# Kernel tuning notes

Measured on AMD Instinct MI355X. Metric: run time of the kernel, lower is better.

## Reference

```python
import jax, jax.numpy as jnp
import numpy as np

NUM_EXPERTS = 8
TOP_K = 2
HIDDEN = 2048
INTER = 7168
B, S = 4, 2048


def setup_inputs() -> dict:
    key = jax.random.key(0)
    k0, k1, k2, k3, k4 = jax.random.split(key, 5)
    scale_h = 1.0 / np.sqrt(HIDDEN)
    scale_i = 1.0 / np.sqrt(INTER)
    return {
        "hidden_states": jax.random.normal(k0, (B, S, HIDDEN), dtype=jnp.float32),
        "gate_w": jax.random.normal(k1, (NUM_EXPERTS, HIDDEN), dtype=jnp.float32) * scale_h,
        "w1": jax.random.normal(k2, (NUM_EXPERTS, INTER, HIDDEN), dtype=jnp.float32) * scale_h,
        "w3": jax.random.normal(k3, (NUM_EXPERTS, INTER, HIDDEN), dtype=jnp.float32) * scale_h,
        "w2": jax.random.normal(k4, (NUM_EXPERTS, HIDDEN, INTER), dtype=jnp.float32) * scale_i,
    }


def reference(hidden_states, gate_w, w1, w3, w2):
    orig_shape = hidden_states.shape
    x = hidden_states.reshape(-1, HIDDEN)              # [T, H]

    # Router: gate linear -> softmax -> top-k -> renormalize.
    router_logits = x @ gate_w.T                       # [T, E]
    probs = jax.nn.softmax(router_logits, axis=-1)
    topk_w, topk_idx = jax.lax.top_k(probs, TOP_K)     # [T, K]
    topk_w = topk_w / jnp.sum(topk_w, axis=-1, keepdims=True)

    # Dense combine weights: [T, E] with top-k renormalized weights scattered.
    combine = jnp.sum(
        jax.nn.one_hot(topk_idx, NUM_EXPERTS, dtype=x.dtype) * topk_w[..., None],
        axis=1,
    )                                                   # [T, E]

    out = jnp.zeros_like(x)
    # Fixed small loop over experts (structurally distinct weight matrices);
    # avoids materializing a [T, E, I] intermediate.
    for e in range(NUM_EXPERTS):
        g = jax.nn.silu(x @ w1[e].T)                   # [T, I]
        u = x @ w3[e].T                                # [T, I]
        y = (g * u) @ w2[e].T                          # [T, H]
        out = out + combine[:, e:e + 1] * y

    return out.reshape(orig_shape)
```

## Files before the change

kernel.cpp:

```cpp
#include <hip/hip_runtime.h>
#include <stdint.h>

#define NE    8
#define HID   2048
#define INTER 7168
#define TTOK  8192
#define NT1   (HID / 64)
#define NT2   (INTER / 64)

typedef __bf16 bf16;
typedef bf16 bf16x4 __attribute__((ext_vector_type(4)));
typedef bf16 bf16x8 __attribute__((ext_vector_type(8)));
typedef float f32x4 __attribute__((ext_vector_type(4)));

__device__ __forceinline__ void glds16(const void* g, void* l) {
  __builtin_amdgcn_global_load_lds((__attribute__((address_space(1))) void*)g,
                                   (__attribute__((address_space(3))) void*)l, 16, 0, 0);
}

__global__ void cvtrt_kernel(const float* __restrict__ w1, const float* __restrict__ w3,
                             bf16* __restrict__ wdst,
                             const float* __restrict__ x, const float* __restrict__ gw,
                             bf16* __restrict__ xb,
                             int* __restrict__ topk_e, float* __restrict__ topk_w) {
  const long SEG = (long)NE * INTER * HID;
  if (blockIdx.x < 8192) {
    const int seg = blockIdx.x >> 12;
    const int bid = blockIdx.x & 4095;
    const float* src = seg ? w3 : w1;
    bf16* d = wdst + (size_t)seg * SEG;
    long i = (long)bid * blockDim.x + threadIdx.x;
    const long stride = (long)4096 * blockDim.x;
    for (long j = i * 4; j < SEG; j += stride * 4) {
      float4 v = *(const float4*)(src + j);
      bf16x4 o = {(bf16)v.x, (bf16)v.y, (bf16)v.z, (bf16)v.w};
      *(bf16x4*)(d + j) = o;
    }
    return;
  }
  const int rb = blockIdx.x - 8192;
  const int wid = threadIdx.x >> 6, lane = threadIdx.x & 63;
  const int t = rb * 4 + wid;
  if (t >= TTOK) return;
  const float* xr = x + (size_t)t * HID;
  bf16* xw = xb + (size_t)t * HID;
  float xv[32];
#pragma unroll
  for (int i = 0; i < 32; ++i) xv[i] = xr[lane + 64 * i];
#pragma unroll
  for (int i = 0; i < 32; ++i) xw[lane + 64 * i] = (bf16)xv[i];
  float lg[NE];
#pragma unroll
  for (int e = 0; e < NE; ++e) {
    const float* g = gw + e * HID;
    float s = 0.f;
#pragma unroll
    for (int i = 0; i < 32; ++i) s += xv[i] * g[lane + 64 * i];
#pragma unroll
    for (int off = 32; off; off >>= 1) s += __shfl_down(s, off);
    lg[e] = s;
  }
  if (lane == 0) {
    int i1 = 0;
#pragma unroll
    for (int e = 1; e < NE; ++e) if (lg[e] > lg[i1]) i1 = e;
    int i2 = (i1 == 0) ? 1 : 0;
#pragma unroll
    for (int e = 0; e < NE; ++e) if (e != i2 && e != i1 && lg[e] > lg[i2]) i2 = e;
    float r = __expf(lg[i2] - lg[i1]);
    float wa = 1.f / (1.f + r);
    topk_e[2 * t] = i1; topk_e[2 * t + 1] = i2;
    topk_w[2 * t] = wa; topk_w[2 * t + 1] = 1.f - wa;
  }
}

__global__ void gather_sorted(const int* __restrict__ topk_e, const float* __restrict__ topk_w,
                              int* __restrict__ cnt, int* __restrict__ ltok,
                              float* __restrict__ lw, int* __restrict__ ppos) {
  const int e = blockIdx.x;
  const int tid = threadIdx.x;
  const int lane = tid & 63, wv = tid >> 6;
  __shared__ int wtot[4];
  __shared__ int basesh;
  if (tid == 0) basesh = 0;
  __syncthreads();
  for (int c0 = 0; c0 < TTOK; c0 += 256) {
    const int t = c0 + tid;
    const int e0 = topk_e[2 * t], e1 = topk_e[2 * t + 1];
    const int j = (e0 == e) ? 0 : 1;
    const int flag = (e0 == e) || (e1 == e);
    unsigned long long b = __ballot(flag);
    int wrank = __popcll(b & ((1ULL << lane) - 1ULL));
    if (lane == 63) wtot[wv] = __popcll(b);
    __syncthreads();
    int wbase = 0;
#pragma unroll
    for (int k = 0; k < 4; ++k) if (k < wv) wbase += wtot[k];
    const int total = wtot[0] + wtot[1] + wtot[2] + wtot[3];
    const int pos = basesh + wbase + wrank;
    if (flag) {
      ltok[e * TTOK + pos] = t;
      lw[e * TTOK + pos] = (j == 0) ? topk_w[2 * t] : topk_w[2 * t + 1];
      ppos[2 * t + j] = pos;
    }
    __syncthreads();
    if (tid == 0) basesh += total;
    __syncthreads();
  }
  if (tid == 0) cnt[e] = basesh;
}

__global__ void combine_kernel(const bf16* __restrict__ ybuf, const int* __restrict__ topk_e,
                               const int* __restrict__ ppos, const int* __restrict__ cnt,
                               float* __restrict__ out) {
  __shared__ int pref[NE];
  if (threadIdx.x < NE) {
    int b = 0;
    for (int k = 0; k < (int)threadIdx.x; ++k) b += cnt[k];
    pref[threadIdx.x] = b;
  }
  __syncthreads();
  const int t = blockIdx.x;
  const int col = threadIdx.x * 8;
  const int g0 = pref[topk_e[2 * t]] + ppos[2 * t];
  const int g1 = pref[topk_e[2 * t + 1]] + ppos[2 * t + 1];
  bf16x8 y0 = *(const bf16x8*)(ybuf + (size_t)g0 * HID + col);
  bf16x8 y1 = *(const bf16x8*)(ybuf + (size_t)g1 * HID + col);
  float4 o0, o1;
  o0.x = (float)y0[0] + (float)y1[0]; o0.y = (float)y0[1] + (float)y1[1];
  o0.z = (float)y0[2] + (float)y1[2]; o0.w = (float)y0[3] + (float)y1[3];
  o1.x = (float)y0[4] + (float)y1[4]; o1.y = (float)y0[5] + (float)y1[5];
  o1.z = (float)y0[6] + (float)y1[6]; o1.w = (float)y0[7] + (float)y1[7];
  float4* o = (float4*)(out + (size_t)t * HID + col);
  o[0] = o0; o[1] = o1;
}


#define MFMA(a, b, c) __builtin_amdgcn_mfma_f32_16x16x32_bf16((a), (b), (c), 0, 0, 0)

#define STAGE_A(h, kt) do { int _b = ((kt) & 1) * 32768; size_t _k = (size_t)(kt) * 128; \
    glds16(bA + oA[(h)*2 + 0] + _k, ldsA + _b + (h) * 16384 + d0); \
    glds16(bA + oA[(h)*2 + 1] + _k, ldsA + _b + (h) * 16384 + d1); } while (0)
#define STAGE_B(h, kt) do { int _b = ((kt) & 1) * 32768; size_t _k = (size_t)(kt) * 128; \
    glds16(bB + oB[(h)*2 + 0] + _k, ldsB + _b + (h) * 16384 + d0); \
    glds16(bB + oB[(h)*2 + 1] + _k, ldsB + _b + (h) * 16384 + d1); } while (0)

#define RD_A(mf, ks) (*(const bf16x8*)(ldsA + curb + arow + (mf) * (16 * 128) + ((ks) ? kcol1 : kcol0)))
#define RD_B(nf, ks) (*(const bf16x8*)(ldsB + curb + brow + (nf) * (16 * 128) + ((ks) ? kcol1 : kcol0)))

#define BAR()    __builtin_amdgcn_s_barrier()
#define LGKMC(n) do { asm volatile("s_waitcnt lgkmcnt(" #n ")" ::: "memory"); \
                      __builtin_amdgcn_sched_barrier(0); } while (0)
#define SCHED0() __builtin_amdgcn_sched_barrier(0)

#define Q_MFMA(AM, BM, ACCM, ACCN_OFF) do { \
  __builtin_amdgcn_s_setprio(1); \
  _Pragma("unroll") \
  for (int m = 0; m < 4; ++m) \
    _Pragma("unroll") \
    for (int n = 0; n < 2; ++n) { \
      acc[ACCM + m][ACCN_OFF + n] = MFMA(AM[m][0], BM[n][0], acc[ACCM + m][ACCN_OFF + n]); \
      acc[ACCM + m][ACCN_OFF + n] = MFMA(AM[m][1], BM[n][1], acc[ACCM + m][ACCN_OFF + n]); \
    } \
  __builtin_amdgcn_s_setprio(0); \
} while (0)

__launch_bounds__(512, 2)
__global__ void pass1_kernel(const bf16* __restrict__ xb, const bf16* __restrict__ w1b,
                             const float* __restrict__ w2f, bf16* __restrict__ w2b,
                             bf16* __restrict__ hbuf, const int* __restrict__ cnt,
                             const int* __restrict__ ltok) {
  if (blockIdx.z == NE) {
    const long n4 = (long)NE * HID * INTER / 4;
    long i = (long)(blockIdx.y * gridDim.x + blockIdx.x) * blockDim.x + threadIdx.x;
    const long stride = (long)gridDim.x * gridDim.y * blockDim.x;
    const float4* src = (const float4*)w2f;
    bf16x4* dst = (bf16x4*)w2b;
    for (long j = i; j < n4; j += stride) {
      float4 v = src[j];
      bf16x4 o = {(bf16)v.x, (bf16)v.y, (bf16)v.z, (bf16)v.w};
      dst[j] = o;
    }
    return;
  }
  const int e = blockIdx.z;
  const int c = cnt[e];
  const int tm = blockIdx.y;
  if (tm * 256 >= c) return;
  const int tn = blockIdx.x;
  int be = 0;
#pragma unroll
  for (int k = 0; k < NE; ++k) if (k < e) be += cnt[k];

  __shared__ __align__(16) bf16 sA[2][256 * 64];
  __shared__ __align__(16) bf16 sB[2][256 * 64];
  char* const ldsA = (char*)&sA[0][0];
  char* const ldsB = (char*)&sB[0][0];

  const int tid = threadIdx.x;
  const int r0 = tid >> 3;
  const int ls = (tid & 7) ^ (r0 & 7);
  const int d0 = tid * 16, d1 = (tid + 512) * 16;
  const char* const bA = (const char*)xb;
  const char* const bB = (const char*)w1b;

  uint32_t oA[4], oB[4];
#pragma unroll
  for (int i = 0; i < 4; ++i) {
    int slot = tm * 256 + i * 64 + r0; if (slot >= c) slot = c - 1;
    oA[i] = (uint32_t)((size_t)ltok[e * TTOK + slot] * (HID * 2) + ls * 16);
    int br = i * 64 + r0;
    int w = (br >> 4) & 1;
    int wr = tn * 128 + ((br >> 5) << 4) + (br & 15);
    size_t off = ((size_t)e * INTER + wr) * (HID * 2) + (size_t)ls * 16;
    if (w) off += (size_t)NE * INTER * HID * 2;
    oB[i] = (uint32_t)off;
  }

  const int lane = tid & 63, wid = tid >> 6;
  const int wm = wid >> 2, wn = wid & 3;
  const int ln15 = lane & 15, kq = lane >> 4;
  const int swz = (ln15 & 7) << 4;
  const int kcol0 = (kq * 16) ^ swz;
  const int kcol1 = (64 + kq * 16) ^ swz;
  const int arow = (wm * 128 + ln15) * 128;
  const int brow = (wn * 64 + ln15) * 128;

  f32x4 acc[8][4];
#pragma unroll
  for (int m = 0; m < 8; ++m)
#pragma unroll
    for (int n = 0; n < 4; ++n) acc[m][n] = (f32x4){0.f, 0.f, 0.f, 0.f};

  STAGE_A(0, 0); STAGE_A(1, 0); STAGE_B(0, 0); STAGE_B(1, 0);
  asm volatile("s_waitcnt vmcnt(4)" ::: "memory");
  STAGE_A(0, 1); STAGE_A(1, 1); STAGE_B(0, 1);
  asm volatile("s_waitcnt vmcnt(6)" ::: "memory");
  BAR();

  bf16x8 a0[4][2], a1[4][2], b0[2][2], b1[2][2];
  int cur = 0;
  for (int t = 0; t < NT1; ++t, cur ^= 1) {
    const int curb = cur * 32768;
#pragma unroll
    for (int m = 0; m < 4; ++m) { a0[m][0] = RD_A(m, 0); a0[m][1] = RD_A(m, 1); }
#pragma unroll
    for (int n = 0; n < 2; ++n) { b0[n][0] = RD_B(n, 0); b0[n][1] = RD_B(n, 1); }
    if (t + 1 < NT1) STAGE_B(1, t + 1);
    BAR(); LGKMC(12);
    if (t > 0) Q_MFMA(a1, b1, 4, 2);
    BAR();
#pragma unroll
    for (int m = 0; m < 4; ++m) { a1[m][0] = RD_A(4 + m, 0); a1[m][1] = RD_A(4 + m, 1); }
    BAR(); LGKMC(8);
    Q_MFMA(a0, b0, 0, 0);
    BAR();
#pragma unroll
    for (int n = 0; n < 2; ++n) { b1[n][0] = RD_B(2 + n, 0); b1[n][1] = RD_B(2 + n, 1); }
    if (t + 2 < NT1) { STAGE_A(0, t + 2); STAGE_A(1, t + 2); SCHED0(); }
    BAR(); LGKMC(4);
    Q_MFMA(a1, b0, 4, 0);
    BAR();
    if (t + 2 < NT1) STAGE_B(0, t + 2);
    LGKMC(0);
    Q_MFMA(a0, b1, 0, 2);
    if (t + 2 < NT1) asm volatile("s_waitcnt vmcnt(6)" ::: "memory");
    else             asm volatile("s_waitcnt vmcnt(0)" ::: "memory");
    BAR();
  }
  Q_MFMA(a1, b1, 4, 2);

#pragma unroll
  for (int mh = 0; mh < 2; ++mh)
#pragma unroll
    for (int mf = 0; mf < 4; ++mf)
#pragma unroll
      for (int j = 0; j < 4; ++j) {
        const int slot = tm * 256 + wm * 128 + mh * 64 + mf * 16 + kq * 4 + j;
        if (slot < c) {
          bf16* hrow = hbuf + (size_t)(be + slot) * INTER + tn * 128;
#pragma unroll
          for (int p = 0; p < 2; ++p) {
            const float g = acc[mh * 4 + mf][2 * p][j];
            const float u = acc[mh * 4 + mf][2 * p + 1][j];
            const float hv = g / (1.f + __expf(-g)) * u;
            hrow[wn * 32 + p * 16 + ln15] = (bf16)hv;
          }
        }
      }
}

__launch_bounds__(512, 2)
__global__ void pass2_kernel(const bf16* __restrict__ hbuf, const bf16* __restrict__ w2b,
                             bf16* __restrict__ ybuf, const int* __restrict__ cnt,
                             const float* __restrict__ lw) {
  const int e = blockIdx.z;
  const int c = cnt[e];
  const int tm = blockIdx.y;
  if (tm * 256 >= c) return;
  const int tn = blockIdx.x;
  int be = 0;
#pragma unroll
  for (int k = 0; k < NE; ++k) if (k < e) be += cnt[k];

  __shared__ __align__(16) bf16 sA[2][256 * 64];
  __shared__ __align__(16) bf16 sB[2][256 * 64];
  char* const ldsA = (char*)&sA[0][0];
  char* const ldsB = (char*)&sB[0][0];

  const int tid = threadIdx.x;
  const int r0 = tid >> 3;
  const int ls = (tid & 7) ^ (r0 & 7);
  const int d0 = tid * 16, d1 = (tid + 512) * 16;
  const char* const bA = (const char*)hbuf;
  const char* const bB = (const char*)w2b;

  uint32_t oA[4], oB[4];
#pragma unroll
  for (int i = 0; i < 4; ++i) {
    int slot = tm * 256 + i * 64 + r0; if (slot >= c) slot = c - 1;
    oA[i] = (uint32_t)((size_t)(be + slot) * (INTER * 2) + ls * 16);
    oB[i] = (uint32_t)(((size_t)e * HID + tn * 256 + i * 64 + r0) * (INTER * 2) + (size_t)ls * 16);
  }

  const int lane = tid & 63, wid = tid >> 6;
  const int wm = wid >> 2, wn = wid & 3;
  const int ln15 = lane & 15, kq = lane >> 4;
  const int swz = (ln15 & 7) << 4;
  const int kcol0 = (kq * 16) ^ swz;
  const int kcol1 = (64 + kq * 16) ^ swz;
  const int arow = (wm * 128 + ln15) * 128;
  const int brow = (wn * 64 + ln15) * 128;

  f32x4 acc[8][4];
#pragma unroll
  for (int m = 0; m < 8; ++m)
#pragma unroll
    for (int n = 0; n < 4; ++n) acc[m][n] = (f32x4){0.f, 0.f, 0.f, 0.f};

  STAGE_A(0, 0); STAGE_A(1, 0); STAGE_B(0, 0); STAGE_B(1, 0);
  asm volatile("s_waitcnt vmcnt(4)" ::: "memory");
  STAGE_A(0, 1); STAGE_A(1, 1); STAGE_B(0, 1);
  asm volatile("s_waitcnt vmcnt(6)" ::: "memory");
  BAR();

  bf16x8 a0[4][2], a1[4][2], b0[2][2], b1[2][2];
  int cur = 0;
  for (int t = 0; t < NT2; ++t, cur ^= 1) {
    const int curb = cur * 32768;
#pragma unroll
    for (int m = 0; m < 4; ++m) { a0[m][0] = RD_A(m, 0); a0[m][1] = RD_A(m, 1); }
#pragma unroll
    for (int n = 0; n < 2; ++n) { b0[n][0] = RD_B(n, 0); b0[n][1] = RD_B(n, 1); }
    if (t + 1 < NT2) STAGE_B(1, t + 1);
    BAR(); LGKMC(12);
    if (t > 0) Q_MFMA(a1, b1, 4, 2);
    BAR();
#pragma unroll
    for (int m = 0; m < 4; ++m) { a1[m][0] = RD_A(4 + m, 0); a1[m][1] = RD_A(4 + m, 1); }
    BAR(); LGKMC(8);
    Q_MFMA(a0, b0, 0, 0);
    BAR();
#pragma unroll
    for (int n = 0; n < 2; ++n) { b1[n][0] = RD_B(2 + n, 0); b1[n][1] = RD_B(2 + n, 1); }
    if (t + 2 < NT2) { STAGE_A(0, t + 2); STAGE_A(1, t + 2); SCHED0(); }
    BAR(); LGKMC(4);
    Q_MFMA(a1, b0, 4, 0);
    BAR();
    if (t + 2 < NT2) STAGE_B(0, t + 2);
    LGKMC(0);
    Q_MFMA(a0, b1, 0, 2);
    if (t + 2 < NT2) asm volatile("s_waitcnt vmcnt(6)" ::: "memory");
    else             asm volatile("s_waitcnt vmcnt(0)" ::: "memory");
    BAR();
  }
  Q_MFMA(a1, b1, 4, 2);

#pragma unroll
  for (int mh = 0; mh < 2; ++mh)
#pragma unroll
    for (int mf = 0; mf < 4; ++mf)
#pragma unroll
      for (int j = 0; j < 4; ++j) {
        const int slot = tm * 256 + wm * 128 + mh * 64 + mf * 16 + kq * 4 + j;
        if (slot < c) {
          const float wt = lw[e * TTOK + slot];
          bf16* yrow = ybuf + (size_t)(be + slot) * HID + tn * 256;
#pragma unroll
          for (int n = 0; n < 4; ++n)
            yrow[wn * 64 + n * 16 + ln15] = (bf16)(wt * acc[mh * 4 + mf][n][j]);
        }
      }
}

extern "C" void kernel_launch(void* const* d_in, const int* in_sizes, int n_in,
                              void* d_out, int out_size, void* d_ws, size_t ws_size,
                              hipStream_t stream) {
  const float* x  = (const float*)d_in[0];
  const float* gw = (const float*)d_in[1];
  const float* w1 = (const float*)d_in[2];
  const float* w3 = (const float*)d_in[3];
  const float* w2 = (const float*)d_in[4];
  float* out = (float*)d_out;

  char* ws = (char*)d_ws;
  size_t off = 0;
  auto take = [&](size_t bytes) -> char* {
    char* p = ws + off;
    off += (bytes + 255) & ~(size_t)255;
    return p;
  };
  bf16* xb    = (bf16*)take((size_t)TTOK * HID * 2);
  bf16* w1b   = (bf16*)take((size_t)NE * INTER * HID * 2);
  bf16* w3b   = (bf16*)take((size_t)NE * INTER * HID * 2);
  bf16* w2b   = (bf16*)take((size_t)NE * HID * INTER * 2);
  bf16* hbuf  = (bf16*)take((size_t)TTOK * 2 * INTER * 2);
  bf16* ybuf  = (bf16*)take((size_t)TTOK * 2 * HID * 2);
  int*   topk_e = (int*)take(TTOK * 2 * 4);
  float* topk_w = (float*)take(TTOK * 2 * 4);
  int*   ltok   = (int*)take(NE * TTOK * 4);
  float* lwgt   = (float*)take(NE * TTOK * 4);
  int*   ppos   = (int*)take(TTOK * 2 * 4);
  int*   cntp   = (int*)take(64);
  if (off > ws_size) return;
  (void)w3b;

  cvtrt_kernel<<<8192 + TTOK / 4, 256, 0, stream>>>(w1, w3, w1b, x, gw, xb, topk_e, topk_w);
  gather_sorted<<<NE, 256, 0, stream>>>(topk_e, topk_w, cntp, ltok, lwgt, ppos);

  pass1_kernel<<<dim3(INTER / 128, TTOK / 256, NE + 1), 512, 0, stream>>>(
      xb, w1b, w2, w2b, hbuf, cntp, ltok);
  pass2_kernel<<<dim3(HID / 256, TTOK / 256, NE), 512, 0, stream>>>(
      hbuf, w2b, ybuf, cntp, lwgt);
  combine_kernel<<<TTOK, 256, 0, stream>>>(ybuf, topk_e, ppos, cntp, out);
}
```

Baseline: 2.105 ms.

## Switch expert GEMMs to 32x32x16 MFMA with k-major LDS layout

Both expert GEMM kernels move from 16x16x32 bf16 MFMA to 32x32x16 bf16 MFMA with 16-wide accumulators. The LDS tile layout becomes k-chunk-major, so each lane reads 16-byte fragments without the XOR swizzle. The main loop becomes a simpler two-phase schedule with full lgkm waits. Larger MFMA tiles aim to cut LDS read traffic per FLOP and instruction count. In exchange, the interleaved multi-phase overlap is gone, and the new layout may cause LDS bank conflicts.

```diff
diff --git a/kernel.cpp b/kernel.cpp
--- a/kernel.cpp
+++ b/kernel.cpp
@@ -11,7 +11,7 @@
 typedef __bf16 bf16;
 typedef bf16 bf16x4 __attribute__((ext_vector_type(4)));
 typedef bf16 bf16x8 __attribute__((ext_vector_type(8)));
-typedef float f32x4 __attribute__((ext_vector_type(4)));
+typedef float f32x16 __attribute__((ext_vector_type(16)));
 
 __device__ __forceinline__ void glds16(const void* g, void* l) {
   __builtin_amdgcn_global_load_lds((__attribute__((address_space(1))) void*)g,
@@ -136,7 +136,7 @@
 }
 
 
-#define MFMA(a, b, c) __builtin_amdgcn_mfma_f32_16x16x32_bf16((a), (b), (c), 0, 0, 0)
+#define MFMA32(a, b, c) __builtin_amdgcn_mfma_f32_32x32x16_bf16((a), (b), (c), 0, 0, 0)
 
 #define STAGE_A(h, kt) do { int _b = ((kt) & 1) * 32768; size_t _k = (size_t)(kt) * 128; \
     glds16(bA + oA[(h)*2 + 0] + _k, ldsA + _b + (h) * 16384 + d0); \
@@ -145,23 +145,23 @@
     glds16(bB + oB[(h)*2 + 0] + _k, ldsB + _b + (h) * 16384 + d0); \
     glds16(bB + oB[(h)*2 + 1] + _k, ldsB + _b + (h) * 16384 + d1); } while (0)
 
-#define RD_A(mf, ks) (*(const bf16x8*)(ldsA + curb + arow + (mf) * (16 * 128) + ((ks) ? kcol1 : kcol0)))
-#define RD_B(nf, ks) (*(const bf16x8*)(ldsB + curb + brow + (nf) * (16 * 128) + ((ks) ? kcol1 : kcol0)))
+#define RD_A(mf, ks) (*(const bf16x8*)(ldsA + curb + aOff + (mf) * 4096 + kcq[ks]))
+#define RD_B(nf, ks) (*(const bf16x8*)(ldsB + curb + bOff + (nf) * 4096 + kcq[ks]))
 
 #define BAR()    __builtin_amdgcn_s_barrier()
-#define LGKMC(n) do { asm volatile("s_waitcnt lgkmcnt(" #n ")" ::: "memory"); \
+#define LGKM0()  do { asm volatile("s_waitcnt lgkmcnt(0)" ::: "memory"); \
                       __builtin_amdgcn_sched_barrier(0); } while (0)
 #define SCHED0() __builtin_amdgcn_sched_barrier(0)
 
-#define Q_MFMA(AM, BM, ACCM, ACCN_OFF) do { \
+#define Q_MFMA32(AM, ACCM) do { \
   __builtin_amdgcn_s_setprio(1); \
   _Pragma("unroll") \
-  for (int m = 0; m < 4; ++m) \
+  for (int ks = 0; ks < 4; ++ks) \
     _Pragma("unroll") \
-    for (int n = 0; n < 2; ++n) { \
-      acc[ACCM + m][ACCN_OFF + n] = MFMA(AM[m][0], BM[n][0], acc[ACCM + m][ACCN_OFF + n]); \
-      acc[ACCM + m][ACCN_OFF + n] = MFMA(AM[m][1], BM[n][1], acc[ACCM + m][ACCN_OFF + n]); \
-    } \
+    for (int m = 0; m < 2; ++m) \
+      _Pragma("unroll") \
+      for (int n = 0; n < 2; ++n) \
+        acc[ACCM + m][n] = MFMA32(AM[m][ks], bF[n][ks], acc[ACCM + m][n]); \
   __builtin_amdgcn_s_setprio(0); \
 } while (0)
 
@@ -198,96 +198,93 @@
   char* const ldsB = (char*)&sB[0][0];
 
   const int tid = threadIdx.x;
-  const int r0 = tid >> 3;
-  const int ls = (tid & 7) ^ (r0 & 7);
   const int d0 = tid * 16, d1 = (tid + 512) * 16;
   const char* const bA = (const char*)xb;
   const char* const bB = (const char*)w1b;
 
   uint32_t oA[4], oB[4];
 #pragma unroll
-  for (int i = 0; i < 4; ++i) {
-    int slot = tm * 256 + i * 64 + r0; if (slot >= c) slot = c - 1;
-    oA[i] = (uint32_t)((size_t)ltok[e * TTOK + slot] * (HID * 2) + ls * 16);
-    int br = i * 64 + r0;
-    int w = (br >> 4) & 1;
-    int wr = tn * 128 + ((br >> 5) << 4) + (br & 15);
-    size_t off = ((size_t)e * INTER + wr) * (HID * 2) + (size_t)ls * 16;
-    if (w) off += (size_t)NE * INTER * HID * 2;
-    oB[i] = (uint32_t)off;
+  for (int j = 0; j < 2; ++j) {
+    const int ch = j ? (tid + 512) : tid;
+    const int g = ch >> 8, q = (ch >> 5) & 7, r = ch & 31;
+#pragma unroll
+    for (int h = 0; h < 2; ++h) {
+      const int rowt = h * 128 + g * 32 + r;
+      int slot = tm * 256 + rowt; if (slot >= c) slot = c - 1;
+      oA[h * 2 + j] = (uint32_t)((size_t)ltok[e * TTOK + slot] * (HID * 2) + q * 16);
+      const int br = rowt;
+      const int w = (br >> 5) & 1;
+      const int wr = tn * 128 + (br >> 6) * 32 + (br & 31);
+      size_t off = ((size_t)e * INTER + wr) * (HID * 2) + (size_t)q * 16;
+      if (w) off += (size_t)NE * INTER * HID * 2;
+      oB[h * 2 + j] = (uint32_t)off;
+    }
   }
 
   const int lane = tid & 63, wid = tid >> 6;
   const int wm = wid >> 2, wn = wid & 3;
-  const int ln15 = lane & 15, kq = lane >> 4;
-  const int swz = (ln15 & 7) << 4;
-  const int kcol0 = (kq * 16) ^ swz;
-  const int kcol1 = (64 + kq * 16) ^ swz;
-  const int arow = (wm * 128 + ln15) * 128;
-  const int brow = (wn * 64 + ln15) * 128;
-
-  f32x4 acc[8][4];
-#pragma unroll
-  for (int m = 0; m < 8; ++m)
-#pragma unroll
-    for (int n = 0; n < 4; ++n) acc[m][n] = (f32x4){0.f, 0.f, 0.f, 0.f};
+  const int ln31 = lane & 31, kq2 = lane >> 5;
+  int kcq[4];
+#pragma unroll
+  for (int ks = 0; ks < 4; ++ks) kcq[ks] = (ks * 2 + kq2) * 512;
+  const int aOff = wm * 16384 + ln31 * 16;
+  const int bOff = (wn >> 1) * 16384 + (wn & 1) * 8192 + ln31 * 16;
+
+  f32x16 acc[4][2];
+#pragma unroll
+  for (int m = 0; m < 4; ++m)
+#pragma unroll
+    for (int n = 0; n < 2; ++n) acc[m][n] = (f32x16)(0.f);
 
   STAGE_A(0, 0); STAGE_A(1, 0); STAGE_B(0, 0); STAGE_B(1, 0);
-  asm volatile("s_waitcnt vmcnt(4)" ::: "memory");
   STAGE_A(0, 1); STAGE_A(1, 1); STAGE_B(0, 1);
   asm volatile("s_waitcnt vmcnt(6)" ::: "memory");
   BAR();
 
-  bf16x8 a0[4][2], a1[4][2], b0[2][2], b1[2][2];
+  bf16x8 aF[2][4], bF[2][4];
   int cur = 0;
   for (int t = 0; t < NT1; ++t, cur ^= 1) {
     const int curb = cur * 32768;
 #pragma unroll
-    for (int m = 0; m < 4; ++m) { a0[m][0] = RD_A(m, 0); a0[m][1] = RD_A(m, 1); }
-#pragma unroll
-    for (int n = 0; n < 2; ++n) { b0[n][0] = RD_B(n, 0); b0[n][1] = RD_B(n, 1); }
-    if (t + 1 < NT1) STAGE_B(1, t + 1);
-    BAR(); LGKMC(12);
-    if (t > 0) Q_MFMA(a1, b1, 4, 2);
-    BAR();
-#pragma unroll
-    for (int m = 0; m < 4; ++m) { a1[m][0] = RD_A(4 + m, 0); a1[m][1] = RD_A(4 + m, 1); }
-    BAR(); LGKMC(8);
-    Q_MFMA(a0, b0, 0, 0);
-    BAR();
-#pragma unroll
-    for (int n = 0; n < 2; ++n) { b1[n][0] = RD_B(2 + n, 0); b1[n][1] = RD_B(2 + n, 1); }
-    if (t + 2 < NT1) { STAGE_A(0, t + 2); STAGE_A(1, t + 2); SCHED0(); }
-    BAR(); LGKMC(4);
-    Q_MFMA(a1, b0, 4, 0);
-    BAR();
-    if (t + 2 < NT1) STAGE_B(0, t + 2);
-    LGKMC(0);
-    Q_MFMA(a0, b1, 0, 2);
+    for (int m = 0; m < 2; ++m)
+#pragma unroll
+      for (int ks = 0; ks < 4; ++ks) aF[m][ks] = RD_A(m, ks);
+#pragma unroll
+    for (int n = 0; n < 2; ++n)
+#pragma unroll
+      for (int ks = 0; ks < 4; ++ks) bF[n][ks] = RD_B(n, ks);
+    LGKM0();
+    BAR();
+    if (t + 1 < NT1) { STAGE_B(1, t + 1); SCHED0(); }
+    Q_MFMA32(aF, 0);
+    BAR();
+#pragma unroll
+    for (int m = 0; m < 2; ++m)
+#pragma unroll
+      for (int ks = 0; ks < 4; ++ks) aF[m][ks] = RD_A(2 + m, ks);
+    LGKM0();
+    BAR();
+    if (t + 2 < NT1) { STAGE_A(0, t + 2); STAGE_A(1, t + 2); STAGE_B(0, t + 2); SCHED0(); }
+    Q_MFMA32(aF, 2);
     if (t + 2 < NT1) asm volatile("s_waitcnt vmcnt(6)" ::: "memory");
     else             asm volatile("s_waitcnt vmcnt(0)" ::: "memory");
     BAR();
   }
-  Q_MFMA(a1, b1, 4, 2);
-
-#pragma unroll
-  for (int mh = 0; mh < 2; ++mh)
-#pragma unroll
-    for (int mf = 0; mf < 4; ++mf)
-#pragma unroll
-      for (int j = 0; j < 4; ++j) {
-        const int slot = tm * 256 + wm * 128 + mh * 64 + mf * 16 + kq * 4 + j;
-        if (slot < c) {
-          bf16* hrow = hbuf + (size_t)(be + slot) * INTER + tn * 128;
-#pragma unroll
-          for (int p = 0; p < 2; ++p) {
-            const float g = acc[mh * 4 + mf][2 * p][j];
-            const float u = acc[mh * 4 + mf][2 * p + 1][j];
-            const float hv = g / (1.f + __expf(-g)) * u;
-            hrow[wn * 32 + p * 16 + ln15] = (bf16)hv;
-          }
-        }
+
+  const int hcol = tn * 128 + wn * 32 + ln31;
+#pragma unroll
+  for (int mf = 0; mf < 4; ++mf)
+#pragma unroll
+    for (int reg = 0; reg < 16; ++reg) {
+      const int row = mf * 32 + (reg & 3) + 8 * (reg >> 2) + 4 * kq2;
+      const int slot = tm * 256 + wm * 128 + row;
+      if (slot < c) {
+        const float g = acc[mf][0][reg];
+        const float u = acc[mf][1][reg];
+        const float hv = g / (1.f + __expf(-g)) * u;
+        hbuf[(size_t)(be + slot) * INTER + hcol] = (bf16)hv;
       }
+    }
 }
 
 __launch_bounds__(512, 2)
@@ -309,88 +306,88 @@
   char* const ldsB = (char*)&sB[0][0];
 
   const int tid = threadIdx.x;
-  const int r0 = tid >> 3;
-  const int ls = (tid & 7) ^ (r0 & 7);
   const int d0 = tid * 16, d1 = (tid + 512) * 16;
   const char* const bA = (const char*)hbuf;
   const char* const bB = (const char*)w2b;
 
   uint32_t oA[4], oB[4];
 #pragma unroll
-  for (int i = 0; i < 4; ++i) {
-    int slot = tm * 256 + i * 64 + r0; if (slot >= c) slot = c - 1;
-    oA[i] = (uint32_t)((size_t)(be + slot) * (INTER * 2) + ls * 16);
-    oB[i] = (uint32_t)(((size_t)e * HID + tn * 256 + i * 64 + r0) * (INTER * 2) + (size_t)ls * 16);
+  for (int j = 0; j < 2; ++j) {
+    const int ch = j ? (tid + 512) : tid;
+    const int g = ch >> 8, q = (ch >> 5) & 7, r = ch & 31;
+#pragma unroll
+    for (int h = 0; h < 2; ++h) {
+      const int rowt = h * 128 + g * 32 + r;
+      int slot = tm * 256 + rowt; if (slot >= c) slot = c - 1;
+      oA[h * 2 + j] = (uint32_t)((size_t)(be + slot) * (INTER * 2) + q * 16);
+      oB[h * 2 + j] = (uint32_t)(((size_t)e * HID + tn * 256 + rowt) * (INTER * 2) + (size_t)q * 16);
+    }
   }
 
   const int lane = tid & 63, wid = tid >> 6;
   const int wm = wid >> 2, wn = wid & 3;
-  const int ln15 = lane & 15, kq = lane >> 4;
-  const int swz = (ln15 & 7) << 4;
-  const int kcol0 = (kq * 16) ^ swz;
-  const int kcol1 = (64 + kq * 16) ^ swz;
-  const int arow = (wm * 128 + ln15) * 128;
-  const int brow = (wn * 64 + ln15) * 128;
-
-  f32x4 acc[8][4];
-#pragma unroll
-  for (int m = 0; m < 8; ++m)
-#pragma unroll
-    for (int n = 0; n < 4; ++n) acc[m][n] = (f32x4){0.f, 0.f, 0.f, 0.f};
+  const int ln31 = lane & 31, kq2 = lane >> 5;
+  int kcq[4];
+#pragma unroll
+  for (int ks = 0; ks < 4; ++ks) kcq[ks] = (ks * 2 + kq2) * 512;
+  const int aOff = wm * 16384 + ln31 * 16;
+  const int bOff = (wn >> 1) * 16384 + (wn & 1) * 8192 + ln31 * 16;
+
+  f32x16 acc[4][2];
+#pragma unroll
+  for (int m = 0; m < 4; ++m)
+#pragma unroll
+    for (int n = 0; n < 2; ++n) acc[m][n] = (f32x16)(0.f);
 
   STAGE_A(0, 0); STAGE_A(1, 0); STAGE_B(0, 0); STAGE_B(1, 0);
-  asm volatile("s_waitcnt vmcnt(4)" ::: "memory");
   STAGE_A(0, 1); STAGE_A(1, 1); STAGE_B(0, 1);
   asm volatile("s_waitcnt vmcnt(6)" ::: "memory");
   BAR();
 
-  bf16x8 a0[4][2], a1[4][2], b0[2][2], b1[2][2];
+  bf16x8 aF[2][4], bF[2][4];
   int cur = 0;
   for (int t = 0; t < NT2; ++t, cur ^= 1) {
     const int curb = cur * 32768;
 #pragma unroll
-    for (int m = 0; m < 4; ++m) { a0[m][0] = RD_A(m, 0); a0[m][1] = RD_A(m, 1); }
-#pragma unroll
-    for (int n = 0; n < 2; ++n) { b0[n][0] = RD_B(n, 0); b0[n][1] = RD_B(n, 1); }
-    if (t + 1 < NT2) STAGE_B(1, t + 1);
-    BAR(); LGKMC(12);
-    if (t > 0) Q_MFMA(a1, b1, 4, 2);
-    BAR();
-#pragma unroll
-    for (int m = 0; m < 4; ++m) { a1[m][0] = RD_A(4 + m, 0); a1[m][1] = RD_A(4 + m, 1); }
-    BAR(); LGKMC(8);
-    Q_MFMA(a0, b0, 0, 0);
-    BAR();
-#pragma unroll
-    for (int n = 0; n < 2; ++n) { b1[n][0] = RD_B(2 + n, 0); b1[n][1] = RD_B(2 + n, 1); }
-    if (t + 2 < NT2) { STAGE_A(0, t + 2); STAGE_A(1, t + 2); SCHED0(); }
-    BAR(); LGKMC(4);
-    Q_MFMA(a1, b0, 4, 0);
-    BAR();
-    if (t + 2 < NT2) STAGE_B(0, t + 2);
-    LGKMC(0);
-    Q_MFMA(a0, b1, 0, 2);
+    for (int m = 0; m < 2; ++m)
+#pragma unroll
+      for (int ks = 0; ks < 4; ++ks) aF[m][ks] = RD_A(m, ks);
+#pragma unroll
+    for (int n = 0; n < 2; ++n)
+#pragma unroll
+      for (int ks = 0; ks < 4; ++ks) bF[n][ks] = RD_B(n, ks);
+    LGKM0();
+    BAR();
+    if (t + 1 < NT2) { STAGE_B(1, t + 1); SCHED0(); }
+    Q_MFMA32(aF, 0);
+    BAR();
+#pragma unroll
+    for (int m = 0; m < 2; ++m)
+#pragma unroll
+      for (int ks = 0; ks < 4; ++ks) aF[m][ks] = RD_A(2 + m, ks);
+    LGKM0();
+    BAR();
+    if (t + 2 < NT2) { STAGE_A(0, t + 2); STAGE_A(1, t + 2); STAGE_B(0, t + 2); SCHED0(); }
+    Q_MFMA32(aF, 2);
     if (t + 2 < NT2) asm volatile("s_waitcnt vmcnt(6)" ::: "memory");
     else             asm volatile("s_waitcnt vmcnt(0)" ::: "memory");
     BAR();
   }
-  Q_MFMA(a1, b1, 4, 2);
-
-#pragma unroll
-  for (int mh = 0; mh < 2; ++mh)
-#pragma unroll
-    for (int mf = 0; mf < 4; ++mf)
-#pragma unroll
-      for (int j = 0; j < 4; ++j) {
-        const int slot = tm * 256 + wm * 128 + mh * 64 + mf * 16 + kq * 4 + j;
-        if (slot < c) {
-          const float wt = lw[e * TTOK + slot];
-          bf16* yrow = ybuf + (size_t)(be + slot) * HID + tn * 256;
-#pragma unroll
-          for (int n = 0; n < 4; ++n)
-            yrow[wn * 64 + n * 16 + ln15] = (bf16)(wt * acc[mh * 4 + mf][n][j]);
-        }
+
+#pragma unroll
+  for (int mf = 0; mf < 4; ++mf)
+#pragma unroll
+    for (int reg = 0; reg < 16; ++reg) {
+      const int row = mf * 32 + (reg & 3) + 8 * (reg >> 2) + 4 * kq2;
+      const int slot = tm * 256 + wm * 128 + row;
+      if (slot < c) {
+        const float wt = lw[e * TTOK + slot];
+        bf16* yrow = ybuf + (size_t)(be + slot) * HID + tn * 256 + wn * 64;
+#pragma unroll
+        for (int nf = 0; nf < 2; ++nf)
+          yrow[nf * 32 + ln31] = (bf16)(wt * acc[mf][nf][reg]);
       }
+    }
 }
 
 extern "C" void kernel_launch(void* const* d_in, const int* in_sizes, int n_in,
```

New measurement: 2.824 ms. +34.2%, slower.
